# Optimization experiments

Hardware: AMD Instinct MI355X
Metric: run time of the kernel (lower is better)

## Reference

```python
import jax, jax.numpy as jnp
import numpy as np

CUTOFF = 5.0
BOX_L = 60.0  # positions are scaled into a 60 A cube


def setup_inputs() -> dict:
    key = jax.random.key(0)
    N = 4096
    xyz = jax.random.uniform(key, (N, 3), dtype=jnp.float32) * BOX_L
    return {"xyz": xyz}


def reference(xyz):
    # All unordered pairs i<j (exclude_ii=True, no periodic box)
    N = xyz.shape[0]
    ii, jj = jnp.triu_indices(N, k=1)            # [P], P = N*(N-1)/2
    deltas = xyz[ii] - xyz[jj]                    # [P, 3]
    dist = jnp.sqrt(jnp.sum(deltas * deltas, axis=-1))  # [P]
    mask = dist < CUTOFF                          # within-cutoff pairs

    # jit-friendly equivalent of the torch NaN-mask compaction:
    # invalid pairs get index -1, zero delta/distance; n_pairs counts valid.
    pair_i = jnp.where(mask, ii, -1).astype(jnp.int32)
    pair_j = jnp.where(mask, jj, -1).astype(jnp.int32)
    pair_diff = jnp.where(mask[:, None], deltas, 0.0)
    pair_dist = jnp.where(mask, dist, 0.0)
    n_pairs = jnp.sum(mask).astype(jnp.int32).reshape(1)
    return pair_i, pair_j, pair_diff, pair_dist, n_pairs
```

## Files before the change

kernel.cpp:

```cpp
#include <hip/hip_runtime.h>


typedef float f4 __attribute__((ext_vector_type(4)));

#define NBLK 2048

__global__ void zero_ws(int* __restrict__ ws, int n) {
    int t = blockIdx.x * blockDim.x + threadIdx.x;
    if (t < n) ws[t] = 0;
}

__global__ __launch_bounds__(256) void nl_kernel(const float* __restrict__ xyz,
                                                 float* __restrict__ out,
                                                 int* __restrict__ ws,
                                                 int N, int P, int slots) {
    const int gsize = (int)gridDim.x * 256;
    const int span = gsize * 4;
    int cnt = 0;

    for (int it_base = 0; it_base < P; it_base += span) {
        const int p0 = it_base + ((int)blockIdx.x * 256 + (int)threadIdx.x) * 4;
        if (p0 >= P) break;

        const int twoNm1 = 2 * N - 1;
        const long long rad = (long long)twoNm1 * twoNm1 - 8LL * (long long)p0;
        const float s = sqrtf((float)rad);
        int i = (int)(((float)twoNm1 - s) * 0.5f);
        if (i > N - 2) i = N - 2;
        if (i < 0) i = 0;
        int rs = i * (2 * N - 1 - i) / 2;
        while (p0 < rs) { --i; rs -= (N - 1 - i); }
        int next = rs + (N - 1 - i);
        while (p0 >= next && i < N - 2) { ++i; rs = next; next += (N - 1 - i); }

        float iv[4], jv[4], dxs[4], dys[4], dzs[4], dv[4];
        #pragma unroll
        for (int e = 0; e < 4; ++e) {
            const int p = p0 + e;
            while (p >= next && i < N - 2) { ++i; rs = next; next += (N - 1 - i); }
            const int j = i + 1 + (p - rs);
            float dx = 0.f, dy = 0.f, dz = 0.f, dist = 0.f, fi = -1.f, fj = -1.f;
            if (p < P) {
                const float ax = xyz[3 * i], ay = xyz[3 * i + 1], az = xyz[3 * i + 2];
                const float bx = xyz[3 * j], by = xyz[3 * j + 1], bz = xyz[3 * j + 2];
                const float tx = ax - bx, ty = ay - by, tz = az - bz;
                const float d = sqrtf(tx * tx + ty * ty + tz * tz);
                if (d < 5.0f) {
                    fi = (float)i; fj = (float)j;
                    dx = tx; dy = ty; dz = tz; dist = d;
                    ++cnt;
                }
            }
            iv[e] = fi; jv[e] = fj; dxs[e] = dx; dys[e] = dy; dzs[e] = dz; dv[e] = dist;
        }

        if (p0 + 4 <= P) {
            *(f4*)(out + p0)     = (f4){iv[0], iv[1], iv[2], iv[3]};
            *(f4*)(out + P + p0) = (f4){jv[0], jv[1], jv[2], jv[3]};
            f4* dp = (f4*)(out + 2 * P + 3 * p0);
            dp[0] = (f4){dxs[0], dys[0], dzs[0], dxs[1]};
            dp[1] = (f4){dys[1], dzs[1], dxs[2], dys[2]};
            dp[2] = (f4){dzs[2], dxs[3], dys[3], dzs[3]};
            *(f4*)(out + 5 * P + p0) = (f4){dv[0], dv[1], dv[2], dv[3]};
        } else {
            for (int e = 0; e < 4 && p0 + e < P; ++e) {
                const int p = p0 + e;
                out[p] = iv[e]; out[P + p] = jv[e];
                out[2 * P + 3 * p]     = dxs[e];
                out[2 * P + 3 * p + 1] = dys[e];
                out[2 * P + 3 * p + 2] = dzs[e];
                out[5 * P + p] = dv[e];
            }
        }
    }

    for (int o = 32; o > 0; o >>= 1) cnt += __shfl_down(cnt, o, 64);
    __shared__ int sh[4];
    if ((threadIdx.x & 63) == 0) sh[threadIdx.x >> 6] = cnt;
    __syncthreads();
    if (threadIdx.x == 0) {
        const int c = sh[0] + sh[1] + sh[2] + sh[3];
        if ((int)gridDim.x <= slots) ws[blockIdx.x] = c;
        else if (c) atomicAdd(&ws[blockIdx.x % slots], c);
    }
}

__global__ void finalize_kernel(float* __restrict__ out, const int* __restrict__ ws,
                                int n, int pos) {
    const int t = threadIdx.x;
    int s = 0;
    for (int k = t; k < n; k += 256) s += ws[k];
    for (int o = 32; o > 0; o >>= 1) s += __shfl_down(s, o, 64);
    __shared__ int sh[4];
    if ((t & 63) == 0) sh[t >> 6] = s;
    __syncthreads();
    if (t == 0) out[pos] = (float)(sh[0] + sh[1] + sh[2] + sh[3]);
}

extern "C" void kernel_launch(void* const* d_in, const int* in_sizes, int n_in,
                              void* d_out, int out_size, void* d_ws, size_t ws_size,
                              hipStream_t stream) {
    const float* xyz = (const float*)d_in[0];
    float* out = (float*)d_out;
    int* ws = (int*)d_ws;

    const int N = in_sizes[0] / 3;
    const int P = (int)((long long)N * (N - 1) / 2);

    const int cap = (int)(ws_size / 4);
    const int slots = (NBLK <= cap) ? NBLK : (cap < 1 ? 1 : cap);
    if (NBLK > slots) zero_ws<<<(slots + 255) / 256, 256, 0, stream>>>(ws, slots);

    nl_kernel<<<NBLK, 256, 0, stream>>>(xyz, out, ws, N, P, slots);
    finalize_kernel<<<1, 256, 0, stream>>>(out, ws, slots, 6 * P);
}
```

Baseline: 43.44 us.

## Fuse count finalization into main kernel via last-block atomic counters

```diff
diff --git a/kernel.cpp b/kernel.cpp
--- a/kernel.cpp
+++ b/kernel.cpp
@@ -2,8 +2,6 @@
 
 
 typedef float f4 __attribute__((ext_vector_type(4)));
-
-#define NBLK 2048
 
 __global__ void zero_ws(int* __restrict__ ws, int n) {
     int t = blockIdx.x * blockDim.x + threadIdx.x;
@@ -12,76 +10,92 @@
 
 __global__ __launch_bounds__(256) void nl_kernel(const float* __restrict__ xyz,
                                                  float* __restrict__ out,
-                                                 int* __restrict__ ws,
-                                                 int N, int P, int slots) {
-    const int gsize = (int)gridDim.x * 256;
-    const int span = gsize * 4;
+                                                 unsigned long long* __restrict__ wsll,
+                                                 int* __restrict__ ws32,
+                                                 int N, int P, int q, int slots) {
+    const int tid = (int)threadIdx.x;
+    int p0 = (int)blockIdx.x * 4096 + tid * 4;
     int cnt = 0;
 
-    for (int it_base = 0; it_base < P; it_base += span) {
-        const int p0 = it_base + ((int)blockIdx.x * 256 + (int)threadIdx.x) * 4;
-        if (p0 >= P) break;
-
-        const int twoNm1 = 2 * N - 1;
+    const int twoNm1 = 2 * N - 1;
+    {
         const long long rad = (long long)twoNm1 * twoNm1 - 8LL * (long long)p0;
         const float s = sqrtf((float)rad);
-        int i = (int)(((float)twoNm1 - s) * 0.5f);
-        if (i > N - 2) i = N - 2;
-        if (i < 0) i = 0;
-        int rs = i * (2 * N - 1 - i) / 2;
-        while (p0 < rs) { --i; rs -= (N - 1 - i); }
-        int next = rs + (N - 1 - i);
-        while (p0 >= next && i < N - 2) { ++i; rs = next; next += (N - 1 - i); }
+        int ii = (int)(((float)twoNm1 - s) * 0.5f);
+        if (ii > N - 2) ii = N - 2;
+        if (ii < 0) ii = 0;
+        int rs = ii * (2 * N - 1 - ii) / 2;
+        while (p0 < rs) { --ii; rs -= (N - 1 - ii); }
+        int next = rs + (N - 1 - ii);
+        while (p0 >= next && ii < N - 2) { ++ii; rs = next; next += (N - 1 - ii); }
 
-        float iv[4], jv[4], dxs[4], dys[4], dzs[4], dv[4];
         #pragma unroll
-        for (int e = 0; e < 4; ++e) {
-            const int p = p0 + e;
-            while (p >= next && i < N - 2) { ++i; rs = next; next += (N - 1 - i); }
-            const int j = i + 1 + (p - rs);
-            float dx = 0.f, dy = 0.f, dz = 0.f, dist = 0.f, fi = -1.f, fj = -1.f;
-            if (p < P) {
-                const float ax = xyz[3 * i], ay = xyz[3 * i + 1], az = xyz[3 * i + 2];
-                const float bx = xyz[3 * j], by = xyz[3 * j + 1], bz = xyz[3 * j + 2];
-                const float tx = ax - bx, ty = ay - by, tz = az - bz;
-                const float d = sqrtf(tx * tx + ty * ty + tz * tz);
-                if (d < 5.0f) {
-                    fi = (float)i; fj = (float)j;
-                    dx = tx; dy = ty; dz = tz; dist = d;
-                    ++cnt;
+        for (int g = 0; g < 4; ++g, p0 += 1024) {
+            if (p0 >= P) break;
+            while (p0 >= next && ii < N - 2) { ++ii; rs = next; next += (N - 1 - ii); }
+
+            float iv[4], jv[4], dxs[4], dys[4], dzs[4], dv[4];
+            #pragma unroll
+            for (int e = 0; e < 4; ++e) {
+                const int p = p0 + e;
+                while (p >= next && ii < N - 2) { ++ii; rs = next; next += (N - 1 - ii); }
+                const int j = ii + 1 + (p - rs);
+                float dx = 0.f, dy = 0.f, dz = 0.f, dist = 0.f, fi = -1.f, fj = -1.f;
+                if (p < P) {
+                    const float ax = xyz[3 * ii], ay = xyz[3 * ii + 1], az = xyz[3 * ii + 2];
+                    const float bx = xyz[3 * j],  by = xyz[3 * j + 1],  bz = xyz[3 * j + 2];
+                    const float tx = ax - bx, ty = ay - by, tz = az - bz;
+                    const float d = sqrtf(tx * tx + ty * ty + tz * tz);
+                    if (d < 5.0f) {
+                        fi = (float)ii; fj = (float)j;
+                        dx = tx; dy = ty; dz = tz; dist = d;
+                        ++cnt;
+                    }
                 }
+                iv[e] = fi; jv[e] = fj; dxs[e] = dx; dys[e] = dy; dzs[e] = dz; dv[e] = dist;
             }
-            iv[e] = fi; jv[e] = fj; dxs[e] = dx; dys[e] = dy; dzs[e] = dz; dv[e] = dist;
-        }
 
-        if (p0 + 4 <= P) {
-            *(f4*)(out + p0)     = (f4){iv[0], iv[1], iv[2], iv[3]};
-            *(f4*)(out + P + p0) = (f4){jv[0], jv[1], jv[2], jv[3]};
-            f4* dp = (f4*)(out + 2 * P + 3 * p0);
-            dp[0] = (f4){dxs[0], dys[0], dzs[0], dxs[1]};
-            dp[1] = (f4){dys[1], dzs[1], dxs[2], dys[2]};
-            dp[2] = (f4){dzs[2], dxs[3], dys[3], dzs[3]};
-            *(f4*)(out + 5 * P + p0) = (f4){dv[0], dv[1], dv[2], dv[3]};
-        } else {
-            for (int e = 0; e < 4 && p0 + e < P; ++e) {
-                const int p = p0 + e;
-                out[p] = iv[e]; out[P + p] = jv[e];
-                out[2 * P + 3 * p]     = dxs[e];
-                out[2 * P + 3 * p + 1] = dys[e];
-                out[2 * P + 3 * p + 2] = dzs[e];
-                out[5 * P + p] = dv[e];
+            if (p0 + 4 <= P) {
+                *(f4*)(out + p0)     = (f4){iv[0], iv[1], iv[2], iv[3]};
+                *(f4*)(out + P + p0) = (f4){jv[0], jv[1], jv[2], jv[3]};
+                f4* dp = (f4*)(out + 2 * P + 3 * p0);
+                dp[0] = (f4){dxs[0], dys[0], dzs[0], dxs[1]};
+                dp[1] = (f4){dys[1], dzs[1], dxs[2], dys[2]};
+                dp[2] = (f4){dzs[2], dxs[3], dys[3], dzs[3]};
+                *(f4*)(out + 5 * P + p0) = (f4){dv[0], dv[1], dv[2], dv[3]};
+            } else {
+                for (int e = 0; e < 4 && p0 + e < P; ++e) {
+                    const int p = p0 + e;
+                    out[p] = iv[e]; out[P + p] = jv[e];
+                    out[2 * P + 3 * p]     = dxs[e];
+                    out[2 * P + 3 * p + 1] = dys[e];
+                    out[2 * P + 3 * p + 2] = dzs[e];
+                    out[5 * P + p] = dv[e];
+                }
             }
         }
     }
 
     for (int o = 32; o > 0; o >>= 1) cnt += __shfl_down(cnt, o, 64);
     __shared__ int sh[4];
-    if ((threadIdx.x & 63) == 0) sh[threadIdx.x >> 6] = cnt;
+    if ((tid & 63) == 0) sh[tid >> 6] = cnt;
     __syncthreads();
-    if (threadIdx.x == 0) {
-        const int c = sh[0] + sh[1] + sh[2] + sh[3];
-        if ((int)gridDim.x <= slots) ws[blockIdx.x] = c;
-        else if (c) atomicAdd(&ws[blockIdx.x % slots], c);
+    if (tid == 0) {
+        const unsigned int c = (unsigned int)(sh[0] + sh[1] + sh[2] + sh[3]);
+        if (q > 0) {
+            unsigned long long old =
+                atomicAdd(&wsll[blockIdx.x & 63], (unsigned long long)c + (1ull << 32));
+            if ((old >> 32) == (unsigned long long)(q - 1)) {
+                const unsigned long long slot_total = (old & 0xffffffffull) + c;
+                unsigned long long old2 =
+                    atomicAdd(&wsll[64], slot_total + (1ull << 32));
+                if ((old2 >> 32) == 63ull)
+                    out[6 * P] = (float)((old2 & 0xffffffffull) + slot_total);
+            }
+        } else {
+            if ((int)gridDim.x <= slots) ws32[blockIdx.x] = (int)c;
+            else if (c) atomicAdd(&ws32[blockIdx.x % slots], (int)c);
+        }
     }
 }
 
@@ -102,15 +116,22 @@
                               hipStream_t stream) {
     const float* xyz = (const float*)d_in[0];
     float* out = (float*)d_out;
-    int* ws = (int*)d_ws;
 
     const int N = in_sizes[0] / 3;
     const int P = (int)((long long)N * (N - 1) / 2);
+    const int nb = (P + 4095) / 4096;
 
-    const int cap = (int)(ws_size / 4);
-    const int slots = (NBLK <= cap) ? NBLK : (cap < 1 ? 1 : cap);
-    if (NBLK > slots) zero_ws<<<(slots + 255) / 256, 256, 0, stream>>>(ws, slots);
-
-    nl_kernel<<<NBLK, 256, 0, stream>>>(xyz, out, ws, N, P, slots);
-    finalize_kernel<<<1, 256, 0, stream>>>(out, ws, slots, 6 * P);
+    if ((nb & 63) == 0 && ws_size >= 65 * sizeof(unsigned long long)) {
+        hipMemsetAsync(d_ws, 0, 65 * sizeof(unsigned long long), stream);
+        nl_kernel<<<nb, 256, 0, stream>>>(xyz, out, (unsigned long long*)d_ws,
+                                          (int*)d_ws, N, P, nb >> 6, 0);
+    } else {
+        int* ws32 = (int*)d_ws;
+        const int cap = (int)(ws_size / 4);
+        const int slots = (nb <= cap) ? nb : (cap < 1 ? 1 : cap);
+        if (nb > slots) zero_ws<<<(slots + 255) / 256, 256, 0, stream>>>(ws32, slots);
+        nl_kernel<<<nb, 256, 0, stream>>>(xyz, out, (unsigned long long*)d_ws,
+                                          ws32, N, P, 0, slots);
+        finalize_kernel<<<1, 256, 0, stream>>>(out, ws32, slots, 6 * P);
+    }
 }
```

New measurement: 48.23 us. 11.0% more time.
